# Kernel optimization log

Hardware: AMD Instinct MI355X
Metric: run time of the kernel (lower is better)

The kernel has to match this reference:

```python
import jax, jax.numpy as jnp
import numpy as np

D_MODEL = 2048
D_INNER = 4096      # expand * d_model
HEADDIM = 64
NHEADS = 64         # d_inner // headdim
D_STATE = 128
NGROUPS = 1
D_CONV = 4
CHUNK = 128
EPS = 1e-5
BATCH = 2
SEQLEN = 4096
D_CONV_CH = D_INNER + 2 * NGROUPS * D_STATE            # 4352
D_IN_PROJ = 2 * D_INNER + 2 * NGROUPS * D_STATE + NHEADS  # 8512


def setup_inputs() -> dict:
    ks = jax.random.split(jax.random.key(0), 9)
    u = jax.random.normal(ks[0], (BATCH, SEQLEN, D_MODEL), jnp.float32)
    W_in = jax.random.normal(ks[1], (D_MODEL, D_IN_PROJ), jnp.float32) * 0.02
    conv_w = jax.random.normal(ks[2], (D_CONV_CH, D_CONV), jnp.float32) * 0.2
    conv_b = jax.random.normal(ks[3], (D_CONV_CH,), jnp.float32) * 0.02
    dt_bias = jax.random.normal(ks[4], (NHEADS,), jnp.float32) * 0.1
    A_log = jax.random.normal(ks[5], (NHEADS,), jnp.float32) * 0.1
    D = jnp.ones((NHEADS,), jnp.float32)
    norm_w = jnp.ones((D_INNER,), jnp.float32)
    W_out = jax.random.normal(ks[8], (D_INNER, D_MODEL), jnp.float32) * 0.02
    return dict(u=u, W_in=W_in, conv_w=conv_w, conv_b=conv_b, dt_bias=dt_bias,
                A_log=A_log, D=D, norm_w=norm_w, W_out=W_out)


def _mamba2_forward(u, W_in, conv_w, conv_b, dt_bias, A_log, D, norm_w, W_out):
    b, L, _ = u.shape
    zxbcdt = u @ W_in                                       # (b, L, 8512)
    z = zxbcdt[..., :D_INNER]
    xBC = zxbcdt[..., D_INNER:D_INNER + D_CONV_CH]
    dt = zxbcdt[..., D_INNER + D_CONV_CH:]                  # (b, L, h)

    # causal depthwise conv1d (padding = d_conv-1, truncated to L) + SiLU
    padded = jnp.pad(xBC, ((0, 0), (D_CONV - 1, 0), (0, 0)))
    xBC_conv = conv_b + sum(padded[:, k:k + L, :] * conv_w[:, k] for k in range(D_CONV))
    xBC_act = jax.nn.silu(xBC_conv)

    x = xBC_act[..., :D_INNER].reshape(b, L, NHEADS, HEADDIM)
    Bm = xBC_act[..., D_INNER:D_INNER + NGROUPS * D_STATE].reshape(b, L, NGROUPS, D_STATE)
    Cm = xBC_act[..., D_INNER + NGROUPS * D_STATE:].reshape(b, L, NGROUPS, D_STATE)
    rep = NHEADS // NGROUPS
    Bh = jnp.repeat(Bm, rep, axis=2)                        # (b, L, h, n)
    Ch = jnp.repeat(Cm, rep, axis=2)

    A = -jnp.exp(A_log)                                     # (h,), negative
    dtf = jax.nn.softplus(dt + dt_bias)                     # (b, L, h)

    # ---- chunked SSD (structured state-space duality) scan ----
    nc = L // CHUNK
    xc = x.reshape(b, nc, CHUNK, NHEADS, HEADDIM)
    Bc = Bh.reshape(b, nc, CHUNK, NHEADS, D_STATE)
    Cc = Ch.reshape(b, nc, CHUNK, NHEADS, D_STATE)
    dtc = dtf.reshape(b, nc, CHUNK, NHEADS)
    cum = jnp.cumsum(dtc * A, axis=2)                       # (b, nc, cs, h), decreasing

    # intra-chunk causal decay matrix L_ij = exp(cum_i - cum_j), i >= j
    idx = jnp.arange(CHUNK)
    mask = (idx[:, None] >= idx[None, :])[None, None, :, :, None]
    seg = cum[:, :, :, None, :] - cum[:, :, None, :, :]     # (b, nc, i, j, h)
    decay = jnp.exp(jnp.where(mask, seg, -jnp.inf))
    CB = jnp.einsum('bcihn,bcjhn->bcijh', Cc, Bc)
    Y_diag = jnp.einsum('bcijh,bcjh,bcjhp->bcihp', CB * decay, dtc, xc)

    # per-chunk final states: sum_j exp(cum_last - cum_j) * dt_j * B_j (x) x_j
    decay_last = jnp.exp(cum[:, :, -1:, :] - cum)           # (b, nc, cs, h)
    states = jnp.einsum('bclh,bclhn,bclhp->bchpn', decay_last * dtc, Bc, xc)

    # inter-chunk recurrence: carry_{c+1} = exp(sum dA_c) * carry_c + states_c
    Atot = jnp.exp(cum[:, :, -1, :])                        # (b, nc, h)
    def step(carry, inp):
        a, s = inp
        return a[..., None, None] * carry + s, carry
    init = jnp.zeros((b, NHEADS, HEADDIM, D_STATE), jnp.float32)
    _, prev = jax.lax.scan(step, init, (jnp.moveaxis(Atot, 1, 0), jnp.moveaxis(states, 1, 0)))
    prev = jnp.moveaxis(prev, 0, 1)                         # (b, nc, h, p, n) state entering each chunk

    Y_off = jnp.einsum('bclhn,bclh,bchpn->bclhp', Cc, jnp.exp(cum), prev)

    y = (Y_diag + Y_off).reshape(b, L, NHEADS, HEADDIM) + D[:, None] * x
    y = y.reshape(b, L, D_INNER)

    # gated RMSNorm: rmsnorm(y * silu(z)) * norm_w
    t = y * jax.nn.silu(z)
    t = t * jax.lax.rsqrt(jnp.mean(t * t, axis=-1, keepdims=True) + EPS) * norm_w
    return t @ W_out


def reference(u, W_in, conv_w, conv_b, dt_bias, A_log, D, norm_w, W_out):
    return _mamba2_forward(u, W_in, conv_w, conv_b, dt_bias, A_log, D, norm_w, W_out)
```

## Files before the change

kernel.cpp:

```cpp
#include <hip/hip_runtime.h>

#define BATCH 2
#define SEQLEN 4096
#define DM 2048
#define DIP 8512
#define DIPP 8576
#define DI 4096
#define DCC 4352
#define NH 64
#define HD 64
#define DSZ 128
#define CHK 128
#define NC 32
#define NBL (BATCH*SEQLEN)
#define LDP 136

typedef __attribute__((ext_vector_type(4))) float f32x4;
typedef __attribute__((ext_vector_type(8))) __bf16 bf16x8;
typedef __attribute__((ext_vector_type(8))) unsigned short us8;
typedef __attribute__((ext_vector_type(4))) unsigned short us4;

__device__ inline float bf2f(unsigned short u){ union{unsigned int i; float f;} v; v.i=((unsigned)u)<<16; return v.f; }
__device__ inline unsigned short f2bf(float f){ union{float f; unsigned int i;} v; v.f=f; unsigned r=(v.i + 0x7FFFu + ((v.i>>16)&1u))>>16; return (unsigned short)r; }

#define GLOAD_LDS16(gp, lp) __builtin_amdgcn_global_load_lds( \
    (const __attribute__((address_space(1))) void*)(gp), \
    (__attribute__((address_space(3))) void*)(lp), 16, 0, 0)

__global__ void beacon_kernel(float* __restrict__ out, float v)
{
    if (blockIdx.x == 0 && threadIdx.x == 0) out[0] = v;
}

__global__ void cast_bf16_kernel(const float* __restrict__ src, unsigned short* __restrict__ dst, size_t n)
{
    size_t stride = (size_t)gridDim.x * blockDim.x * 8;
    for (size_t i = ((size_t)blockIdx.x*blockDim.x + threadIdx.x)*8; i < n; i += stride) {
        float4 a = *(const float4*)&src[i];
        float4 b = *(const float4*)&src[i+4];
        us8 o;
        o[0]=f2bf(a.x); o[1]=f2bf(a.y); o[2]=f2bf(a.z); o[3]=f2bf(a.w);
        o[4]=f2bf(b.x); o[5]=f2bf(b.y); o[6]=f2bf(b.z); o[7]=f2bf(b.w);
        *(us8*)&dst[i] = o;
    }
}

__global__ __launch_bounds__(256) void transpose_cast_kernel(
    const float* __restrict__ in, unsigned short* __restrict__ out, int R, int C)
{
    __shared__ float tile[32][33];
    const int c0 = blockIdx.x*32, r0 = blockIdx.y*32;
    const int tx = threadIdx.x & 31, ty = threadIdx.x >> 5;
    #pragma unroll
    for (int i = 0; i < 4; i++) {
        const int r = r0 + ty + i*8;
        const int c = c0 + tx;
        tile[ty+i*8][tx] = (c < C) ? in[(size_t)r*C + c] : 0.f;
    }
    __syncthreads();
    #pragma unroll
    for (int i = 0; i < 4; i++) {
        const int cc = c0 + ty + i*8;
        const int rr = r0 + tx;
        out[(size_t)cc*R + rr] = f2bf(tile[tx][ty+i*8]);
    }
}

template<int EPI>
__global__ __launch_bounds__(512, 1) void gemm256(
    const unsigned short* __restrict__ A, const unsigned short* __restrict__ Bt,
    float* __restrict__ C, int K, int ldc, int Nmax,
    unsigned short* __restrict__ zbf, unsigned short* __restrict__ xbcbf,
    float* __restrict__ dtf, const float* __restrict__ dt_bias)
{
    __shared__ unsigned short L[65536];
    const int m0 = blockIdx.x * 256;
    const int n0 = blockIdx.y * 256;
    const int tid = threadIdx.x;
    const int lane = tid & 63;
    const int wid  = tid >> 6;
    const int wm = wid >> 2, wn = wid & 3;
    const int lr  = lane & 15;
    const int lkg = (lane >> 4) * 8;
    const int srow = (wid << 4) + (lane >> 3);
    const int scol = ((lane & 7) ^ (lane >> 3)) << 3;
    const int cs0 = lkg ^ ((lr & 7) << 3);
    const int cs1 = cs0 ^ 32;
    const int nt = K >> 6;

    f32x4 acc[8][4];
    #pragma unroll
    for (int i=0;i<8;i++)
        #pragma unroll
        for (int j=0;j<4;j++) acc[i][j] = f32x4{0.f,0.f,0.f,0.f};

    auto stA = [&](int buf, int t, int h) {
        const unsigned short* g = A + (size_t)(m0 + h*128 + srow)*K + t*64 + scol;
        GLOAD_LDS16(g,               &L[buf*32768 + h*8192 + wid*1024]);
        GLOAD_LDS16(g + (size_t)8*K, &L[buf*32768 + h*8192 + wid*1024 + 512]);
    };
    auto stB = [&](int buf, int t, int h) {
        const int rr = n0 + h*128 + srow;
        const int r0 = (rr     > Nmax) ? Nmax : rr;
        const int r1 = (rr + 8 > Nmax) ? Nmax : rr + 8;
        GLOAD_LDS16(Bt + (size_t)r0*K + t*64 + scol, &L[buf*32768 + 16384 + h*8192 + wid*1024]);
        GLOAD_LDS16(Bt + (size_t)r1*K + t*64 + scol, &L[buf*32768 + 16384 + h*8192 + wid*1024 + 512]);
    };
    auto rdA = [&](int buf, int mq, int s, int ks) {
        const int rl = mq*32 + s*16 + lr;
        return *(const bf16x8*)&L[buf*32768 + wm*8192 + rl*64 + (ks ? cs1 : cs0)];
    };
    auto rdB = [&](int buf, int nf, int ks) {
        const int rl = (wn & 1)*64 + nf*16 + lr;
        return *(const bf16x8*)&L[buf*32768 + 16384 + (wn >> 1)*8192 + rl*64 + (ks ? cs1 : cs0)];
    };

    bf16x8 bfr[4][2];
#define PH(BUF, MQ, LOADB, ...) do { \
    bf16x8 af[2][2]; \
    af[0][0]=rdA(BUF,MQ,0,0); af[0][1]=rdA(BUF,MQ,0,1); \
    af[1][0]=rdA(BUF,MQ,1,0); af[1][1]=rdA(BUF,MQ,1,1); \
    if (LOADB) { \
        _Pragma("unroll") \
        for (int nf=0;nf<4;nf++){ bfr[nf][0]=rdB(BUF,nf,0); bfr[nf][1]=rdB(BUF,nf,1);} } \
    __VA_ARGS__; \
    asm volatile("s_barrier" ::: "memory"); \
    __builtin_amdgcn_s_setprio(1); \
    _Pragma("unroll") \
    for (int s=0;s<2;s++) { \
        _Pragma("unroll") \
        for (int nf=0;nf<4;nf++) { \
            acc[(MQ)*2+s][nf] = __builtin_amdgcn_mfma_f32_16x16x32_bf16(af[s][0], bfr[nf][0], acc[(MQ)*2+s][nf], 0,0,0); \
            acc[(MQ)*2+s][nf] = __builtin_amdgcn_mfma_f32_16x16x32_bf16(af[s][1], bfr[nf][1], acc[(MQ)*2+s][nf], 0,0,0); } } \
    __builtin_amdgcn_s_setprio(0); \
} while(0)

    stA(0, 0, 0); stA(0, 0, 1); stB(0, 0, 0); stB(0, 0, 1);
    stB(1, 1, 0); stB(1, 1, 1);
    asm volatile("s_waitcnt vmcnt(4)" ::: "memory");
    asm volatile("s_barrier" ::: "memory");

    #pragma unroll 1
    for (int t = 0; t < nt; t += 2) {
        const int tp2 = (t + 2 < nt) ? t + 2 : nt - 1;
        const int tp3 = (t + 3 < nt) ? t + 3 : nt - 1;
        PH(0, 0, true,  stA(1, t+1, 0));
        PH(0, 1, false, stA(1, t+1, 1));
        PH(0, 2, false, stB(0, tp2, 0));
        PH(0, 3, false, stB(0, tp2, 1); asm volatile("s_waitcnt vmcnt(4)" ::: "memory"));
        PH(1, 0, true,  stA(0, tp2, 0));
        PH(1, 1, false, stA(0, tp2, 1));
        PH(1, 2, false, stB(1, tp3, 0));
        PH(1, 3, false, stB(1, tp3, 1); asm volatile("s_waitcnt vmcnt(4)" ::: "memory"));
    }
#undef PH

    const int cr = (lane >> 4) * 4;
    const int cc = lane & 15;
    #pragma unroll
    for (int i=0;i<8;i++) {
        #pragma unroll
        for (int j=0;j<4;j++) {
            const int row = m0 + wm*128 + i*16 + cr;
            const int col = n0 + wn*64 + j*16 + cc;
            #pragma unroll
            for (int r=0;r<4;r++) {
                const float val = acc[i][j][r];
                const int rr = row + r;
                if (EPI == 0) {
                    C[(size_t)rr*ldc + col] = val;
                } else {
                    if (col < DI) {
                        zbf[(size_t)rr*DI + col] = f2bf(val);
                    } else if (col < DI + DCC) {
                        xbcbf[(size_t)rr*DCC + (col - DI)] = f2bf(val);
                    } else if (col < DI + DCC + NH) {
                        const int hh = col - (DI + DCC);
                        const float x = val + dt_bias[hh];
                        dtf[(size_t)rr*NH + hh] = (x > 20.f) ? x : log1pf(__expf(x));
                    }
                }
            }
        }
    }
}

__global__ __launch_bounds__(256) void conv_x_kernel(
    const unsigned short* __restrict__ xbc,
    const float* __restrict__ cw, const float* __restrict__ cb,
    unsigned short* __restrict__ xT,
    unsigned short* __restrict__ bcbf)
{
    __shared__ float raw[67][68];
    __shared__ unsigned short ot[64][72];
    const int lt = blockIdx.x;
    const int h  = blockIdx.y;
    const int b  = lt >> 6;
    const int l0 = (lt & 63) * 64;
    const int t = threadIdx.x;

    if (h >= 64) {
        const int g4 = h - 64;
        #pragma unroll
        for (int j = 0; j < 2; j++) {
            const int u = t + j*256;
            const int l = u >> 3, pg = (u & 7)*8;
            const int ch0 = DI + g4*64 + pg;
            const int row = b*SEQLEN + l0 + l;
            float a[8];
            #pragma unroll
            for (int e=0;e<8;e++) a[e] = cb[ch0+e];
            #pragma unroll
            for (int k = 0; k < 4; k++) {
                if (l0 + l + k >= 3) {
                    us8 v = *(const us8*)&xbc[(size_t)(row + k - 3)*DCC + ch0];
                    #pragma unroll
                    for (int e=0;e<8;e++) a[e] += bf2f(v[e]) * cw[(ch0+e)*4 + k];
                }
            }
            us8 o;
            #pragma unroll
            for (int e=0;e<8;e++){ const float s = a[e]/(1.f+__expf(-a[e])); o[e]=f2bf(s); }
            *(us8*)&bcbf[(size_t)row*256 + g4*64 + pg] = o;
        }
        return;
    }

    for (int i = t; i < 536; i += 256) {
        const int li = i >> 3, cg = (i & 7) * 8;
        const int l = l0 - 3 + li;
        us8 v;
        #pragma unroll
        for (int e = 0; e < 8; e++) v[e] = 0;
        if (l >= 0) v = *(const us8*)&xbc[(size_t)(b*SEQLEN + l)*DCC + h*64 + cg];
        #pragma unroll
        for (int e = 0; e < 8; e++) raw[li][cg+e] = bf2f(v[e]);
    }
    __syncthreads();
    #pragma unroll
    for (int j = 0; j < 16; j++) {
        const int i = t + j*256;
        const int l = i >> 6, p = i & 63;
        const int ch = h*64 + p;
        float a = cb[ch];
        #pragma unroll
        for (int k = 0; k < 4; k++) a += raw[l + k][p] * cw[ch*4 + k];
        a = a / (1.f + __expf(-a));
        ot[l][p] = f2bf(a);
    }
    __syncthreads();
    for (int i = t; i < 512; i += 256) {
        const int p = i >> 3, lg = (i & 7) * 8;
        us8 o;
        #pragma unroll
        for (int e = 0; e < 8; e++) o[e] = ot[lg + e][p];
        *(us8*)&xT[(size_t)((b*NH + h)*HD + p)*SEQLEN + l0 + lg] = o;
    }
}

__global__ void cum_kernel(const float* __restrict__ dtf, const float* __restrict__ A_log,
                           float* __restrict__ cum)
{
    const int idx = blockIdx.x*blockDim.x + threadIdx.x;
    if (idx >= BATCH*NC*NH) return;
    const int h = idx & 63;
    const int bc = idx >> 6;
    const float A = -__expf(A_log[h]);
    float c = 0.f;
    const float* src = dtf + (size_t)bc*CHK*NH + h;
    float* dst = cum + (size_t)bc*CHK*NH + h;
    for (int i = 0; i < CHK; i++) { c += src[i*NH]*A; dst[i*NH] = c; }
}

__global__ __launch_bounds__(256, 3) void ssm_passS(
    const unsigned short* __restrict__ bcbf,
    const unsigned short* __restrict__ xT,
    const float* __restrict__ cumg,
    const float* __restrict__ dtfg,
    unsigned short* __restrict__ states)
{
    __shared__ unsigned short BT[128*LDP];
    __shared__ float w_s[128];

    const int blk = blockIdx.x;
    const int h = blk & 63;
    const int bc = blk >> 6;
    const int r0 = bc * CHK;
    const int t = threadIdx.x;
    const int lane = t & 63;
    const int wid = t >> 6;

    if (t < 128) {
        const float cl = cumg[(size_t)(r0+127)*NH + h];
        const float ci = cumg[(size_t)(r0+t)*NH + h];
        const float dt = dtfg[(size_t)(r0+t)*NH + h];
        w_s[t] = __expf(cl - ci) * dt;
    }
    for (int i = t; i < 2048; i += 256) {
        const int l = i >> 4, cg = (i & 15)*8;
        us8 v = *(const us8*)(bcbf + (size_t)(r0+l)*256 + cg);
        #pragma unroll
        for (int e = 0; e < 8; e++) BT[(cg+e)*LDP + l] = v[e];
    }
    __syncthreads();

    const int lr = lane & 15;
    const int lkg = (lane >> 4)*8;
    const int wr = wid >> 1, wc = wid & 1;
    const int b = bc >> 5;
    const int li = (bc & 31) * CHK;
    const unsigned short* xb = xT + (size_t)((b*NH + h)*HD)*SEQLEN + li;

    f32x4 acc[2][4];
    #pragma unroll
    for (int i=0;i<2;i++)
        #pragma unroll
        for (int j=0;j<4;j++) acc[i][j] = f32x4{0.f,0.f,0.f,0.f};
    #pragma unroll
    for (int k = 0; k < 4; k++) {
        bf16x8 a[2], bfr[4];
        #pragma unroll
        for (int i=0;i<2;i++) {
            us8 xv = *(const us8*)(xb + (size_t)(wr*32 + i*16 + lr)*SEQLEN + k*32 + lkg);
            us8 aw;
            #pragma unroll
            for (int e=0;e<8;e++) aw[e] = f2bf(bf2f(xv[e]) * w_s[k*32 + lkg + e]);
            a[i] = __builtin_bit_cast(bf16x8, aw);
        }
        #pragma unroll
        for (int j=0;j<4;j++) bfr[j] = *(const bf16x8*)&BT[(wc*64 + j*16 + lr)*LDP + k*32 + lkg];
        #pragma unroll
        for (int i=0;i<2;i++)
            #pragma unroll
            for (int j=0;j<4;j++)
                acc[i][j] = __builtin_amdgcn_mfma_f32_16x16x32_bf16(a[i], bfr[j], acc[i][j], 0,0,0);
    }
    unsigned short* sb = states + (size_t)blk * (HD*DSZ);
    const int cr = (lane >> 4)*4, cc = lane & 15;
    #pragma unroll
    for (int i=0;i<2;i++) {
        #pragma unroll
        for (int j=0;j<4;j++) {
            const int nn = wc*64 + j*16 + cc;
            #pragma unroll
            for (int r=0;r<4;r++) {
                const int pp = wr*32 + i*16 + cr + r;
                sb[pp*DSZ + nn] = f2bf(acc[i][j][r]);
            }
        }
    }
}

__global__ void scan_kernel(unsigned short* __restrict__ states, const float* __restrict__ cumg)
{
    const int idx = blockIdx.x*256 + threadIdx.x;
    const int n = idx & 127;
    const int p = (idx >> 7) & 63;
    const int h = (idx >> 13) & 63;
    const int b = idx >> 19;
    float carry = 0.f;
    for (int c = 0; c < NC; c++) {
        const size_t off = ((size_t)((b*NC + c)*NH + h))*(HD*DSZ) + p*DSZ + n;
        const float s = bf2f(states[off]);
        states[off] = f2bf(carry);
        const float atot = __expf(cumg[(size_t)((b*NC+c)*CHK + 127)*NH + h]);
        carry = atot*carry + s;
    }
}

__global__ __launch_bounds__(256, 3) void ssm_passY(
    const unsigned short* __restrict__ bcbf,
    const unsigned short* __restrict__ xT,
    const unsigned short* __restrict__ statesg,
    const float* __restrict__ cumg,
    const float* __restrict__ dtfg,
    const float* __restrict__ Dg,
    unsigned short* __restrict__ y)
{
    __shared__ unsigned short P1[128*LDP];
    __shared__ float cum_s[128], dtc_s[128];

    const int blk = blockIdx.x;
    const int h = blk & 63;
    const int bc = blk >> 6;
    const int r0 = bc * CHK;
    const int t = threadIdx.x;
    const int lane = t & 63;
    const int wid = t >> 6;

    if (t < 128) {
        cum_s[t] = cumg[(size_t)(r0+t)*NH + h];
        dtc_s[t] = dtfg[(size_t)(r0+t)*NH + h];
    }
    for (int i = t; i < 2048; i += 256) {
        const int l = i >> 4, cg = (i & 15)*8;
        *(us8*)&P1[l*LDP + cg] = *(const us8*)(bcbf + (size_t)(r0+l)*256 + 128 + cg);
    }
    __syncthreads();

    const int lr = lane & 15;
    const int lkg = (lane >> 4)*8;
    const int wr = wid >> 1, wc = wid & 1;
    const int b = bc >> 5;
    const int li = (bc & 31) * CHK;
    const unsigned short* xb = xT + (size_t)((b*NH + h)*HD)*SEQLEN + li;
    const unsigned short* sb = statesg + (size_t)blk * (HD*DSZ);
    const unsigned short* bb = bcbf + (size_t)r0*256;

    f32x4 acc1[4][4], acc2[4][2];
    #pragma unroll
    for (int i=0;i<4;i++) {
        #pragma unroll
        for (int j=0;j<4;j++) acc1[i][j] = f32x4{0.f,0.f,0.f,0.f};
        #pragma unroll
        for (int j=0;j<2;j++) acc2[i][j] = f32x4{0.f,0.f,0.f,0.f};
    }
    #pragma unroll
    for (int k = 0; k < 4; k++) {
        bf16x8 a[4], bfr[4], pv[2];
        #pragma unroll
        for (int i=0;i<4;i++) a[i] = *(const bf16x8*)&P1[(wr*64 + i*16 + lr)*LDP + k*32 + lkg];
        #pragma unroll
        for (int j=0;j<4;j++) bfr[j] = *(const bf16x8*)(bb + (size_t)(wc*64 + j*16 + lr)*256 + k*32 + lkg);
        #pragma unroll
        for (int j=0;j<2;j++) pv[j] = *(const bf16x8*)(sb + (size_t)(wc*32 + j*16 + lr)*DSZ + k*32 + lkg);
        #pragma unroll
        for (int i=0;i<4;i++) {
            #pragma unroll
            for (int j=0;j<4;j++)
                acc1[i][j] = __builtin_amdgcn_mfma_f32_16x16x32_bf16(a[i], bfr[j], acc1[i][j], 0,0,0);
            #pragma unroll
            for (int j=0;j<2;j++)
                acc2[i][j] = __builtin_amdgcn_mfma_f32_16x16x32_bf16(a[i], pv[j], acc2[i][j], 0,0,0);
        }
    }
    __syncthreads();
    const float Dv = Dg[h];
    const int cr = (lane >> 4)*4, cc = lane & 15;
    #pragma unroll
    for (int i=0;i<4;i++) {
        #pragma unroll
        for (int j=0;j<4;j++) {
            const int jj = wc*64 + j*16 + cc;
            #pragma unroll
            for (int r=0;r<4;r++) {
                const int ii = wr*64 + i*16 + cr + r;
                float v = 0.f;
                if (jj <= ii) v = acc1[i][j][r] * __expf(cum_s[ii] - cum_s[jj]) * dtc_s[jj];
                if (jj == ii) v += Dv;
                P1[ii*LDP + jj] = f2bf(v);
            }
        }
    }
    __syncthreads();
    #pragma unroll
    for (int i=0;i<4;i++) {
        #pragma unroll
        for (int r=0;r<4;r++) {
            const int ii = wr*64 + i*16 + cr + r;
            const float sc = __expf(cum_s[ii]);
            #pragma unroll
            for (int j=0;j<2;j++) acc2[i][j][r] *= sc;
        }
    }
    #pragma unroll
    for (int k = 0; k < 4; k++) {
        bf16x8 a[4], x2[2];
        #pragma unroll
        for (int i=0;i<4;i++) a[i] = *(const bf16x8*)&P1[(wr*64 + i*16 + lr)*LDP + k*32 + lkg];
        #pragma unroll
        for (int j=0;j<2;j++) x2[j] = *(const bf16x8*)(xb + (size_t)(wc*32 + j*16 + lr)*SEQLEN + k*32 + lkg);
        #pragma unroll
        for (int i=0;i<4;i++)
            #pragma unroll
            for (int j=0;j<2;j++)
                acc2[i][j] = __builtin_amdgcn_mfma_f32_16x16x32_bf16(a[i], x2[j], acc2[i][j], 0,0,0);
    }
    #pragma unroll
    for (int i=0;i<4;i++) {
        #pragma unroll
        for (int j=0;j<2;j++) {
            const int pp = wc*32 + j*16 + cc;
            #pragma unroll
            for (int r=0;r<4;r++) {
                const int ii = wr*64 + i*16 + cr + r;
                y[(size_t)(r0+ii)*DI + h*64 + pp] = f2bf(acc2[i][j][r]);
            }
        }
    }
}

__global__ __launch_bounds__(256) void gate_rms_kernel(
    const unsigned short* __restrict__ y, const unsigned short* __restrict__ z,
    const float* __restrict__ nw, unsigned short* __restrict__ tbf)
{
    const int row = blockIdx.x;
    const int t = threadIdx.x;
    const int lane = t & 63, wid = t >> 6;
    float tv[16];
    float ss = 0.f;
    #pragma unroll
    for (int i = 0; i < 2; i++) {
        const int c = (i*256 + t)*8;
        const us8 yv = *(const us8*)&y[(size_t)row*DI + c];
        const us8 zv = *(const us8*)&z[(size_t)row*DI + c];
        #pragma unroll
        for (int e = 0; e < 8; e++) {
            const float fy = bf2f(yv[e]);
            const float fz = bf2f(zv[e]);
            const float v = fy * (fz / (1.f + __expf(-fz)));
            tv[i*8+e] = v;
            ss += v*v;
        }
    }
    #pragma unroll
    for (int o = 1; o < 64; o <<= 1) ss += __shfl_xor(ss, o, 64);
    __shared__ float red[4];
    if (lane == 0) red[wid] = ss;
    __syncthreads();
    const float rms = rsqrtf((red[0]+red[1]+red[2]+red[3]) * (1.f/DI) + 1e-5f);
    #pragma unroll
    for (int i = 0; i < 2; i++) {
        const int c = (i*256 + t)*8;
        us8 o;
        #pragma unroll
        for (int e = 0; e < 8; e += 4) {
            const float4 wv = *(const float4*)&nw[c + e];
            o[e+0]=f2bf(tv[i*8+e+0]*rms*wv.x);
            o[e+1]=f2bf(tv[i*8+e+1]*rms*wv.y);
            o[e+2]=f2bf(tv[i*8+e+2]*rms*wv.z);
            o[e+3]=f2bf(tv[i*8+e+3]*rms*wv.w);
        }
        *(us8*)&tbf[(size_t)row*DI + c] = o;
    }
}

extern "C" void kernel_launch(void* const* d_in, const int* in_sizes, int n_in,
                              void* d_out, int out_size, void* d_ws, size_t ws_size,
                              hipStream_t stream)
{
    const float* u       = (const float*)d_in[0];
    const float* W_in    = (const float*)d_in[1];
    const float* conv_w  = (const float*)d_in[2];
    const float* conv_b  = (const float*)d_in[3];
    const float* dt_bias = (const float*)d_in[4];
    const float* A_log   = (const float*)d_in[5];
    const float* Dp      = (const float*)d_in[6];
    const float* norm_w  = (const float*)d_in[7];
    const float* W_out   = (const float*)d_in[8];
    float* out = (float*)d_out;

    char* ws = (char*)d_ws;
    const size_t OFF_WINT = 33554432;
    const size_t OFF_R2   = 68681728;
    const size_t OFF_R3   = 139984896;
    const size_t OFF_SM   = 207093760;
    const size_t NEED     = OFF_SM + 2097152 + 2097152 + 4194304;
    if (ws_size < NEED) {
        beacon_kernel<<<1, 64, 0, stream>>>(out, 10000.f + (float)(ws_size >> 20));
        return;
    }

    unsigned short* u_bf   = (unsigned short*)(ws);
    unsigned short* winT   = (unsigned short*)(ws + OFF_WINT);
    unsigned short* xTb    = (unsigned short*)(ws);
    unsigned short* t_bf   = (unsigned short*)(ws);
    unsigned short* xbc_bf = (unsigned short*)(ws + OFF_R2);
    unsigned short* y_bf   = (unsigned short*)(ws + OFF_R2);
    unsigned short* states = (unsigned short*)(ws + OFF_R3);
    unsigned short* woutT  = (unsigned short*)(ws + OFF_R3);
    float*          dtf    = (float*)(ws + OFF_SM);
    float*          cum    = (float*)(ws + OFF_SM + 2097152);
    unsigned short* bc_bf  = (unsigned short*)(ws + OFF_SM + 4194304);
    unsigned short* z_bf   = (unsigned short*)d_out;

    cast_bf16_kernel<<<2048, 256, 0, stream>>>(u, u_bf, (size_t)NBL*DM);
    transpose_cast_kernel<<<dim3(DIPP/32, DM/32), 256, 0, stream>>>(W_in, winT, DM, DIP);
    gemm256<1><<<dim3(NBL/256, (DIPP+255)/256), 512, 0, stream>>>(
        u_bf, winT, nullptr, DM, 0, DIPP-1, z_bf, xbc_bf, dtf, dt_bias);
    conv_x_kernel<<<dim3(NBL/64, NH+4), 256, 0, stream>>>(xbc_bf, conv_w, conv_b, xTb, bc_bf);
    cum_kernel<<<64, 64, 0, stream>>>(dtf, A_log, cum);
    ssm_passS<<<BATCH*NC*NH, 256, 0, stream>>>(bc_bf, xTb, cum, dtf, states);
    scan_kernel<<<4096, 256, 0, stream>>>(states, cum);
    ssm_passY<<<BATCH*NC*NH, 256, 0, stream>>>(bc_bf, xTb, states, cum, dtf, Dp, y_bf);
    gate_rms_kernel<<<NBL, 256, 0, stream>>>(y_bf, z_bf, norm_w, t_bf);
    transpose_cast_kernel<<<dim3(DM/32, DI/32), 256, 0, stream>>>(W_out, woutT, DI, DM);
    gemm256<0><<<dim3(NBL/256, DM/256), 512, 0, stream>>>(
        t_bf, woutT, out, DI, DM, DM-1, nullptr, nullptr, nullptr, nullptr);
}
```

Before: 834.4 us.

## Cut per-phase GEMM barriers and vectorize weight transpose with 64x64 tiles

In the bf16 MFMA GEMM main loop, the per-phase s_barrier is replaced by one barrier after the first phase of each buffer half plus a waitcnt+barrier at its end. Both A-tile global-to-LDS loads are now issued together up front, so waves stall on barriers less often. The weight transpose-cast kernel moves to 64x64 tiles with float4 global loads and 16-byte bf16 stores, which cuts the transaction count. The risk is that the looser synchronization depends on the reordered LDS writes never overlapping reads in flight.

After: 843.6 us. About the same (+1.1%).

```diff
diff --git a/kernel.cpp b/kernel.cpp
--- a/kernel.cpp
+++ b/kernel.cpp
@@ -48,21 +48,35 @@
 __global__ __launch_bounds__(256) void transpose_cast_kernel(
     const float* __restrict__ in, unsigned short* __restrict__ out, int R, int C)
 {
-    __shared__ float tile[32][33];
-    const int c0 = blockIdx.x*32, r0 = blockIdx.y*32;
-    const int tx = threadIdx.x & 31, ty = threadIdx.x >> 5;
-    #pragma unroll
-    for (int i = 0; i < 4; i++) {
-        const int r = r0 + ty + i*8;
-        const int c = c0 + tx;
-        tile[ty+i*8][tx] = (c < C) ? in[(size_t)r*C + c] : 0.f;
-    }
-    __syncthreads();
-    #pragma unroll
-    for (int i = 0; i < 4; i++) {
-        const int cc = c0 + ty + i*8;
-        const int rr = r0 + tx;
-        out[(size_t)cc*R + rr] = f2bf(tile[tx][ty+i*8]);
+    __shared__ float tile[64][65];
+    const int c0 = blockIdx.x*64, r0 = blockIdx.y*64;
+    const int t = threadIdx.x;
+    const int tx = t & 15;
+    const int ty = t >> 4;
+    if (c0 < C) {
+        #pragma unroll
+        for (int i = 0; i < 4; i++) {
+            const int r = ty + i*16;
+            const float4 v = *(const float4*)&in[(size_t)(r0+r)*C + c0 + tx*4];
+            tile[r][tx*4+0]=v.x; tile[r][tx*4+1]=v.y; tile[r][tx*4+2]=v.z; tile[r][tx*4+3]=v.w;
+        }
+    } else {
+        #pragma unroll
+        for (int i = 0; i < 4; i++) {
+            const int r = ty + i*16;
+            tile[r][tx*4+0]=0.f; tile[r][tx*4+1]=0.f; tile[r][tx*4+2]=0.f; tile[r][tx*4+3]=0.f;
+        }
+    }
+    __syncthreads();
+    const int cl = t >> 3;
+    const int rg = (t & 7) * 8;
+    #pragma unroll
+    for (int j = 0; j < 2; j++) {
+        const int cc = cl + j*32;
+        us8 o;
+        #pragma unroll
+        for (int e = 0; e < 8; e++) o[e] = f2bf(tile[rg+e][cc]);
+        *(us8*)&out[(size_t)(c0+cc)*R + r0 + rg] = o;
     }
 }
 
@@ -116,15 +130,14 @@
     };
 
     bf16x8 bfr[4][2];
-#define PH(BUF, MQ, LOADB, ...) do { \
+#define PH(BUF, MQ, LOADB, PRE, POST) do { \
     bf16x8 af[2][2]; \
     af[0][0]=rdA(BUF,MQ,0,0); af[0][1]=rdA(BUF,MQ,0,1); \
     af[1][0]=rdA(BUF,MQ,1,0); af[1][1]=rdA(BUF,MQ,1,1); \
     if (LOADB) { \
         _Pragma("unroll") \
         for (int nf=0;nf<4;nf++){ bfr[nf][0]=rdB(BUF,nf,0); bfr[nf][1]=rdB(BUF,nf,1);} } \
-    __VA_ARGS__; \
-    asm volatile("s_barrier" ::: "memory"); \
+    PRE; \
     __builtin_amdgcn_s_setprio(1); \
     _Pragma("unroll") \
     for (int s=0;s<2;s++) { \
@@ -133,27 +146,33 @@
             acc[(MQ)*2+s][nf] = __builtin_amdgcn_mfma_f32_16x16x32_bf16(af[s][0], bfr[nf][0], acc[(MQ)*2+s][nf], 0,0,0); \
             acc[(MQ)*2+s][nf] = __builtin_amdgcn_mfma_f32_16x16x32_bf16(af[s][1], bfr[nf][1], acc[(MQ)*2+s][nf], 0,0,0); } } \
     __builtin_amdgcn_s_setprio(0); \
+    POST; \
 } while(0)
+#define NOP do{}while(0)
+#define BAR asm volatile("s_barrier" ::: "memory")
+#define VM4BAR do { asm volatile("s_waitcnt vmcnt(4)" ::: "memory"); asm volatile("s_barrier" ::: "memory"); } while(0)
 
     stA(0, 0, 0); stA(0, 0, 1); stB(0, 0, 0); stB(0, 0, 1);
     stB(1, 1, 0); stB(1, 1, 1);
-    asm volatile("s_waitcnt vmcnt(4)" ::: "memory");
-    asm volatile("s_barrier" ::: "memory");
+    VM4BAR;
 
     #pragma unroll 1
     for (int t = 0; t < nt; t += 2) {
         const int tp2 = (t + 2 < nt) ? t + 2 : nt - 1;
         const int tp3 = (t + 3 < nt) ? t + 3 : nt - 1;
-        PH(0, 0, true,  stA(1, t+1, 0));
-        PH(0, 1, false, stA(1, t+1, 1));
-        PH(0, 2, false, stB(0, tp2, 0));
-        PH(0, 3, false, stB(0, tp2, 1); asm volatile("s_waitcnt vmcnt(4)" ::: "memory"));
-        PH(1, 0, true,  stA(0, tp2, 0));
-        PH(1, 1, false, stA(0, tp2, 1));
-        PH(1, 2, false, stB(1, tp3, 0));
-        PH(1, 3, false, stB(1, tp3, 1); asm volatile("s_waitcnt vmcnt(4)" ::: "memory"));
+        PH(0, 0, true,  stA(1, t+1, 0); stA(1, t+1, 1), BAR);
+        PH(0, 1, false, stB(0, tp2, 0), NOP);
+        PH(0, 2, false, stB(0, tp2, 1), NOP);
+        PH(0, 3, false, NOP, VM4BAR);
+        PH(1, 0, true,  stA(0, tp2, 0); stA(0, tp2, 1), BAR);
+        PH(1, 1, false, stB(1, tp3, 0), NOP);
+        PH(1, 2, false, stB(1, tp3, 1), NOP);
+        PH(1, 3, false, NOP, VM4BAR);
     }
 #undef PH
+#undef NOP
+#undef BAR
+#undef VM4BAR
 
     const int cr = (lane >> 4) * 4;
     const int cc = lane & 15;
@@ -575,7 +594,7 @@
     unsigned short* z_bf   = (unsigned short*)d_out;
 
     cast_bf16_kernel<<<2048, 256, 0, stream>>>(u, u_bf, (size_t)NBL*DM);
-    transpose_cast_kernel<<<dim3(DIPP/32, DM/32), 256, 0, stream>>>(W_in, winT, DM, DIP);
+    transpose_cast_kernel<<<dim3(DIPP/64, DM/64), 256, 0, stream>>>(W_in, winT, DM, DIP);
     gemm256<1><<<dim3(NBL/256, (DIPP+255)/256), 512, 0, stream>>>(
         u_bf, winT, nullptr, DM, 0, DIPP-1, z_bf, xbc_bf, dtf, dt_bias);
     conv_x_kernel<<<dim3(NBL/64, NH+4), 256, 0, stream>>>(xbc_bf, conv_w, conv_b, xTb, bc_bf);
@@ -584,7 +603,7 @@
     scan_kernel<<<4096, 256, 0, stream>>>(states, cum);
     ssm_passY<<<BATCH*NC*NH, 256, 0, stream>>>(bc_bf, xTb, states, cum, dtf, Dp, y_bf);
     gate_rms_kernel<<<NBL, 256, 0, stream>>>(y_bf, z_bf, norm_w, t_bf);
-    transpose_cast_kernel<<<dim3(DM/32, DI/32), 256, 0, stream>>>(W_out, woutT, DI, DM);
+    transpose_cast_kernel<<<dim3(DM/64, DI/64), 256, 0, stream>>>(W_out, woutT, DI, DM);
     gemm256<0><<<dim3(NBL/256, DM/256), 512, 0, stream>>>(
         t_bf, woutT, out, DI, DM, DM-1, nullptr, nullptr, nullptr, nullptr);
 }
```
